# Performance work log

Measured on AMD Instinct MI355X. Metric: run time of the kernel, lower is better.

Reference implementation:

```python
import jax, jax.numpy as jnp
import numpy as np

B, M, FIN, K, FOUT, NNZ = 8, 40000, 64, 6, 64, 320000

def setup_inputs() -> dict:
    key = jax.random.key(0)
    k1, k2, k3, k4, k5 = jax.random.split(key, 5)
    x = jax.random.normal(k1, (B, M, FIN), dtype=jnp.float32)
    edge_rows = jax.random.randint(k2, (NNZ,), 0, M)
    edge_cols = jax.random.randint(k3, (NNZ,), 0, M)
    edge_vals = jax.random.normal(k4, (NNZ,), dtype=jnp.float32) * 0.1
    W = jax.random.normal(k5, (FIN * K, FOUT), dtype=jnp.float32) * 0.05
    return {"x": x, "edge_vals": edge_vals, "W": W,
            "edge_rows": edge_rows, "edge_cols": edge_cols}

def reference(x, edge_vals, W, edge_rows, edge_cols):
    Bd, Md, Fin = x.shape
    nK = W.shape[0] // Fin
    Fout = W.shape[1]
    # x0: [M, Fin*B] as in tf.transpose([1,2,0]) + reshape
    x0 = jnp.transpose(x, (1, 2, 0)).reshape(Md, Fin * Bd)

    def spmm_rescaled(v):
        # rescale_L(L, lmax=2) = L - I, so (L - I) @ v = L@v - v
        Lv = jax.ops.segment_sum(edge_vals[:, None] * v[edge_cols],
                                 edge_rows, num_segments=Md)
        return Lv - v

    xs = [x0]
    if nK > 1:
        x1 = spmm_rescaled(x0)
        xs.append(x1)
        xp, xc = x0, x1
        for _ in range(2, nK):
            xn = 2.0 * spmm_rescaled(xc) - xp  # Chebyshev recurrence
            xs.append(xn)
            xp, xc = xc, xn
    X = jnp.stack(xs, axis=0)                     # [K, M, Fin*B]
    X = X.reshape(nK, Md, Fin, Bd)                # split Fin*B -> (Fin, B)
    X = jnp.transpose(X, (3, 1, 2, 0))            # [B, M, Fin, K]
    X = X.reshape(Bd * Md, Fin * nK)
    out = (X @ W).reshape(Bd, Md, Fout)           # dense projection
    return out
```

## Files before the change

kernel.cpp:

```cpp
#include <hip/hip_runtime.h>

#define Mn    40000
#define Bn    8
#define FINn  64
#define Kn    6
#define FOUTn 64
#define NNZn  320000
#define Cn    512
#define NB    ((Mn + 255) / 256)
#define MT    (Mn / 64)


typedef _Float16 half8 __attribute__((ext_vector_type(8)));
typedef __attribute__((ext_vector_type(4))) float floatx4;

__device__ __forceinline__ ushort f2h(float f) {
    _Float16 h = (_Float16)f;
    return *(ushort*)&h;
}

__device__ __forceinline__ void gl_lds16(const ushort* g, ushort* l) {
    __builtin_amdgcn_global_load_lds(
        (const __attribute__((address_space(1))) unsigned int*)g,
        (__attribute__((address_space(3))) unsigned int*)l, 16, 0, 0);
}


__global__ __launch_bounds__(256) void k_hist(const int* __restrict__ rows,
                                              int* __restrict__ cnt) {
    int e = blockIdx.x * 256 + threadIdx.x;
    if (e < NNZn) atomicAdd(&cnt[rows[e]], 1);
}

__global__ __launch_bounds__(256) void k_scan_part(const int* __restrict__ cnt,
                                                   int* __restrict__ rowptr,
                                                   int* __restrict__ bsum) {
    __shared__ int part[256];
    int tid = threadIdx.x;
    int r = blockIdx.x * 256 + tid;
    int v = (r < Mn) ? cnt[r] : 0;
    part[tid] = v;
    __syncthreads();
    for (int off = 1; off < 256; off <<= 1) {
        int t = (tid >= off) ? part[tid - off] : 0;
        __syncthreads();
        part[tid] += t;
        __syncthreads();
    }
    if (r < Mn) rowptr[r] = part[tid] - v;
    if (tid == 255) bsum[blockIdx.x] = part[255];
}

__global__ __launch_bounds__(256) void k_scan_bsums(const int* __restrict__ bsum,
                                                    int* __restrict__ boff,
                                                    int* __restrict__ rowptr) {
    __shared__ int part[256];
    int tid = threadIdx.x;
    int v = (tid < NB) ? bsum[tid] : 0;
    part[tid] = v;
    __syncthreads();
    for (int off = 1; off < 256; off <<= 1) {
        int t = (tid >= off) ? part[tid - off] : 0;
        __syncthreads();
        part[tid] += t;
        __syncthreads();
    }
    if (tid < NB) boff[tid] = part[tid] - v;
    if (tid == 255) rowptr[Mn] = part[255];
}

__global__ __launch_bounds__(256) void k_scan_add(int* __restrict__ rowptr,
                                                  const int* __restrict__ boff,
                                                  int* __restrict__ wcur) {
    int r = blockIdx.x * 256 + threadIdx.x;
    if (r < Mn) {
        int v = rowptr[r] + boff[blockIdx.x];
        rowptr[r] = v;
        wcur[r] = v;
    }
}

__global__ __launch_bounds__(256) void k_scatter(const int* __restrict__ rows,
                                                 const int* __restrict__ cols,
                                                 const float* __restrict__ vals,
                                                 int* __restrict__ wcur,
                                                 int2* __restrict__ csr) {
    int e = blockIdx.x * 256 + threadIdx.x;
    if (e < NNZn) {
        int p = atomicAdd(&wcur[rows[e]], 1);
        int2 cv; cv.x = cols[e]; cv.y = __float_as_int(vals[e]);
        csr[p] = cv;
    }
}


__global__ __launch_bounds__(256) void k_transpose_h(const float* __restrict__ x,
                                                     ushort* __restrict__ x0h) {
    int m0 = blockIdx.x * 4;
    int t  = threadIdx.x;
#pragma unroll
    for (int k = 0; k < 2; ++k) {
        int i   = t + k * 256;
        int ml  = i >> 7;
        int rem = i & 127;
        int b   = rem >> 4;
        int fq  = (rem & 15) * 4;
        float4 a = *(const float4*)(x + ((size_t)b * Mn + m0 + ml) * 64 + fq);
        union { uint2 u; ushort h[4]; } s;
        s.h[0] = f2h(a.x); s.h[1] = f2h(a.y); s.h[2] = f2h(a.z); s.h[3] = f2h(a.w);
        *(uint2*)(x0h + (size_t)(m0 + ml) * Cn + b * 64 + fq) = s.u;
    }
}


__device__ __forceinline__ void fmah8(float* a, uint4 g, float w) {
    union { uint4 u; _Float16 h[8]; } c; c.u = g;
#pragma unroll
    for (int i = 0; i < 8; ++i) a[i] += w * (float)c.h[i];
}

__global__ __launch_bounds__(256) void k_spmm_h(const ushort* __restrict__ xc,
                                                const ushort* __restrict__ xp,
                                                ushort* __restrict__ xn,
                                                const int* __restrict__ rowptr,
                                                const int2* __restrict__ csr,
                                                int first) {
    int t = threadIdx.x;
    int lane = t & 63;
    int m = blockIdx.x * 4 + (t >> 6);
    const uint4* xc4 = (const uint4*)xc;
    uint4 v = xc4[(size_t)m * 64 + lane];
    uint4 p;
    if (!first) p = ((const uint4*)xp)[(size_t)m * 64 + lane];
    float a[8];
    { union { uint4 u; _Float16 h[8]; } c; c.u = v;
#pragma unroll
      for (int i = 0; i < 8; ++i) a[i] = -(float)c.h[i]; }

    int e = rowptr[m], end = rowptr[m + 1];
    for (; e + 8 <= end; e += 8) {
        int2 cv[8];
#pragma unroll
        for (int i = 0; i < 8; ++i) cv[i] = csr[e + i];
        uint4 g[8];
#pragma unroll
        for (int i = 0; i < 8; ++i) g[i] = xc4[(size_t)cv[i].x * 64 + lane];
#pragma unroll
        for (int i = 0; i < 8; ++i) fmah8(a, g[i], __int_as_float(cv[i].y));
    }
    for (; e + 4 <= end; e += 4) {
        int2 cv0 = csr[e],     cv1 = csr[e + 1];
        int2 cv2 = csr[e + 2], cv3 = csr[e + 3];
        uint4 g0 = xc4[(size_t)cv0.x * 64 + lane];
        uint4 g1 = xc4[(size_t)cv1.x * 64 + lane];
        uint4 g2 = xc4[(size_t)cv2.x * 64 + lane];
        uint4 g3 = xc4[(size_t)cv3.x * 64 + lane];
        fmah8(a, g0, __int_as_float(cv0.y));
        fmah8(a, g1, __int_as_float(cv1.y));
        fmah8(a, g2, __int_as_float(cv2.y));
        fmah8(a, g3, __int_as_float(cv3.y));
    }
    for (; e < end; ++e) {
        int2 cv = csr[e];
        uint4 g = xc4[(size_t)cv.x * 64 + lane];
        fmah8(a, g, __int_as_float(cv.y));
    }

    if (!first) {
        union { uint4 u; _Float16 h[8]; } c; c.u = p;
#pragma unroll
        for (int i = 0; i < 8; ++i) a[i] = 2.f * a[i] - (float)c.h[i];
    }
    union { uint4 u; _Float16 h[8]; } s;
#pragma unroll
    for (int i = 0; i < 8; ++i) s.h[i] = (_Float16)a[i];
    ((uint4*)xn)[(size_t)m * 64 + lane] = s.u;
}


__global__ __launch_bounds__(256) void k_wfrag(const float* __restrict__ W,
                                               ushort* __restrict__ wfrag) {
    int idx = blockIdx.x * 256 + threadIdx.x;
    if (idx >= 12 * 4 * 64 * 8) return;
    int j    = idx & 7;
    int lane = (idx >> 3) & 63;
    int n    = (idx >> 9) & 3;
    int kk   = idx >> 11;
    int k    = (lane >> 4) * 8 + j;
    int lev  = kk >> 1;
    int f    = (kk & 1) * 32 + k;
    int fo   = n * 16 + (lane & 15);
    wfrag[idx] = f2h(W[(f * Kn + lev) * FOUTn + fo]);
}


__global__ __launch_bounds__(256, 4) void k_gemm_mfma(const ushort* __restrict__ xh,
                                                      const ushort* __restrict__ wfrag,
                                                      float* __restrict__ out) {
    __shared__ __align__(16) ushort As[2][4][1024];
    int t     = threadIdx.x;
    int wv    = t >> 6;
    int lane  = t & 63;
    int q     = lane >> 4, r = lane & 15;
    int mtile = blockIdx.x % MT;
    int b     = blockIdx.x / MT;
    int m0    = mtile * 64;

    const size_t lstrideH = (size_t)Mn * Cn;

    int srow = lane >> 3;
    int gsw  = (lane & 7) ^ (srow & 7);
    const ushort* gsA = xh + (size_t)(m0 + wv * 16 + srow) * Cn + b * 64 + gsw * 8;
    const ushort* gsB = gsA + 8 * (size_t)Cn;
    int swz = r & 7;

    floatx4 acc0 = (floatx4)0.f, acc1 = (floatx4)0.f;
    floatx4 acc2 = (floatx4)0.f, acc3 = (floatx4)0.f;

#define STAGE(lev, buf) do {                                       \
        gl_lds16(gsA + (size_t)(lev) * lstrideH, &As[buf][wv][0]);   \
        gl_lds16(gsB + (size_t)(lev) * lstrideH, &As[buf][wv][512]); \
    } while (0)

#define MC(kkg, af) do {                                                              \
        const ushort* wf = wfrag + ((size_t)((kkg) * 4) * 64 + lane) * 8;             \
        acc0 = __builtin_amdgcn_mfma_f32_16x16x32_f16(af, *(const half8*)(wf),        acc0, 0, 0, 0); \
        acc1 = __builtin_amdgcn_mfma_f32_16x16x32_f16(af, *(const half8*)(wf + 512),  acc1, 0, 0, 0); \
        acc2 = __builtin_amdgcn_mfma_f32_16x16x32_f16(af, *(const half8*)(wf + 1024), acc2, 0, 0, 0); \
        acc3 = __builtin_amdgcn_mfma_f32_16x16x32_f16(af, *(const half8*)(wf + 1536), acc3, 0, 0, 0); \
    } while (0)

#define LEVEL(lev, buf, VMSTR) do {                                                   \
        asm volatile("s_waitcnt vmcnt(" VMSTR ")" ::: "memory");                      \
        __builtin_amdgcn_sched_barrier(0);                                            \
        half8 af0 = *(const half8*)&As[buf][wv][r * 64 + (((0 + q) ^ swz) << 3)];     \
        half8 af1 = *(const half8*)&As[buf][wv][r * 64 + (((4 + q) ^ swz) << 3)];     \
        asm volatile("s_waitcnt lgkmcnt(0)" ::: "memory");                            \
        __builtin_amdgcn_sched_barrier(0);                                            \
        if ((lev) < 4) STAGE((lev) + 2, buf);                                         \
        MC((lev) * 2, af0);                                                           \
        MC((lev) * 2 + 1, af1);                                                       \
    } while (0)

    STAGE(0, 0);
    STAGE(1, 1);
    LEVEL(0, 0, "2");
    LEVEL(1, 1, "2");
    LEVEL(2, 0, "2");
    LEVEL(3, 1, "2");
    LEVEL(4, 0, "2");
    LEVEL(5, 1, "0");

#undef LEVEL
#undef MC
#undef STAGE

    size_t obase = ((size_t)b * Mn + m0 + wv * 16) * FOUTn;
#pragma unroll
    for (int n = 0; n < 4; ++n) {
        floatx4 av = (n == 0) ? acc0 : (n == 1) ? acc1 : (n == 2) ? acc2 : acc3;
#pragma unroll
        for (int reg = 0; reg < 4; ++reg) {
            int orow = q * 4 + reg;
            out[obase + (size_t)orow * FOUTn + n * 16 + r] = av[reg];
        }
    }
}


__global__ __launch_bounds__(512) void k_transpose_f(const float* __restrict__ x,
                                                     float* __restrict__ x0) {
    int m = blockIdx.x, t = threadIdx.x;
    int b = t >> 6, f = t & 63;
    x0[(size_t)m * Cn + t] = x[((size_t)b * Mn + m) * 64 + f];
}

__global__ __launch_bounds__(256) void k_spmm_f32(const float4* __restrict__ xc,
                                                  const float4* __restrict__ xp,
                                                  float4* __restrict__ xn,
                                                  const int* __restrict__ rowptr,
                                                  const int2* __restrict__ csr,
                                                  int first) {
    int t = threadIdx.x;
    int lane = t & 63;
    int m = blockIdx.x * 4 + (t >> 6);
    size_t rb = (size_t)m * 128;
    float4 v0 = xc[rb + lane];
    float4 v1 = xc[rb + 64 + lane];
    float4 a0 = make_float4(-v0.x, -v0.y, -v0.z, -v0.w);
    float4 a1 = make_float4(-v1.x, -v1.y, -v1.z, -v1.w);
    int e = rowptr[m], end = rowptr[m + 1];
    for (; e < end; ++e) {
        int2 cv = csr[e];
        float w = __int_as_float(cv.y);
        const float4* r = xc + (size_t)cv.x * 128;
        float4 g0 = r[lane], g1 = r[64 + lane];
        a0.x += w * g0.x; a0.y += w * g0.y; a0.z += w * g0.z; a0.w += w * g0.w;
        a1.x += w * g1.x; a1.y += w * g1.y; a1.z += w * g1.z; a1.w += w * g1.w;
    }
    if (!first) {
        float4 p0 = xp[rb + lane];
        float4 p1 = xp[rb + 64 + lane];
        a0.x = 2.f * a0.x - p0.x; a0.y = 2.f * a0.y - p0.y;
        a0.z = 2.f * a0.z - p0.z; a0.w = 2.f * a0.w - p0.w;
        a1.x = 2.f * a1.x - p1.x; a1.y = 2.f * a1.y - p1.y;
        a1.z = 2.f * a1.z - p1.z; a1.w = 2.f * a1.w - p1.w;
    }
    xn[rb + lane] = a0;
    xn[rb + 64 + lane] = a1;
}

__global__ __launch_bounds__(256) void k_gemm2(const float* __restrict__ xa,
                                               const float* __restrict__ xb,
                                               const float* __restrict__ W,
                                               float* __restrict__ out,
                                               int ka, int kb, int accum) {
    __shared__ __align__(16) float Wa[64 * 64];
    __shared__ __align__(16) float Wb[64 * 64];
    __shared__ __align__(16) float xsa[4 * Cn];
    __shared__ __align__(16) float xsb[4 * Cn];
    int t = threadIdx.x;
    size_t m0 = (size_t)blockIdx.x * 4;
    for (int i = t; i < 4096; i += 256) {
        int f = i >> 6, fo = i & 63;
        Wa[i] = W[(f * Kn + ka) * FOUTn + fo];
        Wb[i] = W[(f * Kn + kb) * FOUTn + fo];
    }
    for (int i = t; i < 4 * Cn; i += 256) {
        xsa[i] = xa[m0 * Cn + i];
        xsb[i] = xb[m0 * Cn + i];
    }
    __syncthreads();
    int fo  = (t & 15) * 4;
    int idx = t >> 4;
    int m   = idx & 3;
    int bq  = idx >> 2;
    float4 acc0 = make_float4(0.f, 0.f, 0.f, 0.f);
    float4 acc1 = make_float4(0.f, 0.f, 0.f, 0.f);
    for (int f = 0; f < 64; ++f) {
        float4 wa = *(const float4*)&Wa[f * 64 + fo];
        float a0 = xsa[m * Cn + bq * 64 + f];
        float a1 = xsa[m * Cn + (bq + 4) * 64 + f];
        acc0.x += a0 * wa.x; acc0.y += a0 * wa.y; acc0.z += a0 * wa.z; acc0.w += a0 * wa.w;
        acc1.x += a1 * wa.x; acc1.y += a1 * wa.y; acc1.z += a1 * wa.z; acc1.w += a1 * wa.w;
        float4 wb = *(const float4*)&Wb[f * 64 + fo];
        float b0 = xsb[m * Cn + bq * 64 + f];
        float b1 = xsb[m * Cn + (bq + 4) * 64 + f];
        acc0.x += b0 * wb.x; acc0.y += b0 * wb.y; acc0.z += b0 * wb.z; acc0.w += b0 * wb.w;
        acc1.x += b1 * wb.x; acc1.y += b1 * wb.y; acc1.z += b1 * wb.z; acc1.w += b1 * wb.w;
    }
    size_t o0 = (((size_t)bq * Mn) + (m0 + m)) * FOUTn + fo;
    size_t o1 = (((size_t)(bq + 4) * Mn) + (m0 + m)) * FOUTn + fo;
    float4* out4_0 = (float4*)&out[o0];
    float4* out4_1 = (float4*)&out[o1];
    if (accum) {
        float4 c0 = *out4_0, c1 = *out4_1;
        acc0.x += c0.x; acc0.y += c0.y; acc0.z += c0.z; acc0.w += c0.w;
        acc1.x += c1.x; acc1.y += c1.y; acc1.z += c1.z; acc1.w += c1.w;
    }
    *out4_0 = acc0;
    *out4_1 = acc1;
}


extern "C" void kernel_launch(void* const* d_in, const int* in_sizes, int n_in,
                              void* d_out, int out_size, void* d_ws, size_t ws_size,
                              hipStream_t stream) {
    const float* x         = (const float*)d_in[0];
    const float* edge_vals = (const float*)d_in[1];
    const float* W         = (const float*)d_in[2];
    const int*   edge_rows = (const int*)d_in[3];
    const int*   edge_cols = (const int*)d_in[4];
    float* out = (float*)d_out;

    char* ws = (char*)d_ws;
    const size_t bufB = (size_t)Mn * Cn * sizeof(float);
    const size_t bufH = (size_t)Mn * Cn * sizeof(ushort);
    const size_t wfB  = 12 * 4 * 64 * 8 * sizeof(ushort);
    const size_t csrB = (size_t)(Mn + 4 + Mn) * 4 + (size_t)NNZn * 8;

    const int spmm_grid = Mn / 4;
    const int gemm_grid = MT * 8;

    if (ws_size >= 6 * bufH + wfB + csrB) {
        ushort* xh  = (ushort*)ws;
        ushort* wfr = (ushort*)(ws + 6 * bufH);
        int*    rowptr = (int*)(ws + 6 * bufH + wfB);
        int*    fill   = rowptr + (Mn + 4);
        int2*   csr    = (int2*)(fill + Mn);
        int*    bsum   = (int*)csr;
        int*    boff   = bsum + 256;
        ushort* slot[6];
        for (int l = 0; l < 6; ++l) slot[l] = xh + (size_t)l * Mn * Cn;

        hipMemsetAsync(fill, 0, Mn * sizeof(int), stream);
        k_hist<<<(NNZn + 255) / 256, 256, 0, stream>>>(edge_rows, fill);
        k_scan_part<<<NB, 256, 0, stream>>>(fill, rowptr, bsum);
        k_scan_bsums<<<1, 256, 0, stream>>>(bsum, boff, rowptr);
        k_scan_add<<<NB, 256, 0, stream>>>(rowptr, boff, fill);
        k_scatter<<<(NNZn + 255) / 256, 256, 0, stream>>>(edge_rows, edge_cols,
                                                          edge_vals, fill, csr);
        k_wfrag<<<96, 256, 0, stream>>>(W, wfr);

        k_transpose_h<<<Mn / 4, 256, 0, stream>>>(x, slot[0]);
        k_spmm_h<<<spmm_grid, 256, 0, stream>>>(slot[0], slot[0], slot[1],
                                                rowptr, csr, 1);
        k_spmm_h<<<spmm_grid, 256, 0, stream>>>(slot[1], slot[0], slot[2],
                                                rowptr, csr, 0);
        k_spmm_h<<<spmm_grid, 256, 0, stream>>>(slot[2], slot[1], slot[3],
                                                rowptr, csr, 0);
        k_spmm_h<<<spmm_grid, 256, 0, stream>>>(slot[3], slot[2], slot[4],
                                                rowptr, csr, 0);
        k_spmm_h<<<spmm_grid, 256, 0, stream>>>(slot[4], slot[3], slot[5],
                                                rowptr, csr, 0);
        k_gemm_mfma<<<gemm_grid, 256, 0, stream>>>(xh, wfr, out);
    } else {
        float* buf0 = (float*)(ws);
        float* buf1 = (float*)(ws + bufB);
        float* buf2 = (float*)(ws + 2 * bufB);
        int*   rowptr = (int*)(ws + 3 * bufB);
        int*   fill   = rowptr + (Mn + 4);
        int2*  csr    = (int2*)(fill + Mn);
        int*   bsum   = (int*)csr;
        int*   boff   = bsum + 256;
        hipMemsetAsync(fill, 0, Mn * sizeof(int), stream);
        k_hist<<<(NNZn + 255) / 256, 256, 0, stream>>>(edge_rows, fill);
        k_scan_part<<<NB, 256, 0, stream>>>(fill, rowptr, bsum);
        k_scan_bsums<<<1, 256, 0, stream>>>(bsum, boff, rowptr);
        k_scan_add<<<NB, 256, 0, stream>>>(rowptr, boff, fill);
        k_scatter<<<(NNZn + 255) / 256, 256, 0, stream>>>(edge_rows, edge_cols,
                                                          edge_vals, fill, csr);
        k_transpose_f<<<Mn, 512, 0, stream>>>(x, buf0);
        k_spmm_f32<<<Mn / 4, 256, 0, stream>>>((const float4*)buf0, (const float4*)buf0,
                                               (float4*)buf1, rowptr, csr, 1);
        k_gemm2<<<Mn / 4, 256, 0, stream>>>(buf0, buf1, W, out, 0, 1, 0);
        k_spmm_f32<<<Mn / 4, 256, 0, stream>>>((const float4*)buf1, (const float4*)buf0,
                                               (float4*)buf2, rowptr, csr, 0);
        k_spmm_f32<<<Mn / 4, 256, 0, stream>>>((const float4*)buf2, (const float4*)buf1,
                                               (float4*)buf0, rowptr, csr, 0);
        k_gemm2<<<Mn / 4, 256, 0, stream>>>(buf2, buf0, W, out, 2, 3, 1);
        k_spmm_f32<<<Mn / 4, 256, 0, stream>>>((const float4*)buf0, (const float4*)buf2,
                                               (float4*)buf1, rowptr, csr, 0);
        k_spmm_f32<<<Mn / 4, 256, 0, stream>>>((const float4*)buf1, (const float4*)buf0,
                                               (float4*)buf2, rowptr, csr, 0);
        k_gemm2<<<Mn / 4, 256, 0, stream>>>(buf1, buf2, W, out, 4, 5, 1);
    }
}
```

Baseline: 540.4 us.

## Repartition GEMM waves by output column so weight fragments stay in registers

```diff
diff --git a/kernel.cpp b/kernel.cpp
--- a/kernel.cpp
+++ b/kernel.cpp
@@ -197,7 +197,7 @@
 __global__ __launch_bounds__(256, 4) void k_gemm_mfma(const ushort* __restrict__ xh,
                                                       const ushort* __restrict__ wfrag,
                                                       float* __restrict__ out) {
-    __shared__ __align__(16) ushort As[2][4][1024];
+    __shared__ __align__(16) ushort As[2][4096];
     int t     = threadIdx.x;
     int wv    = t >> 6;
     int lane  = t & 63;
@@ -205,64 +205,80 @@
     int mtile = blockIdx.x % MT;
     int b     = blockIdx.x / MT;
     int m0    = mtile * 64;
+    int swz   = r & 7;
 
     const size_t lstrideH = (size_t)Mn * Cn;
 
-    int srow = lane >> 3;
+    const ushort* wfb = wfrag + ((size_t)wv * 64 + lane) * 8;
+    half8 wf0  = *(const half8*)(wfb);
+    half8 wf1  = *(const half8*)(wfb + 1 * 2048);
+    half8 wf2  = *(const half8*)(wfb + 2 * 2048);
+    half8 wf3  = *(const half8*)(wfb + 3 * 2048);
+    half8 wf4  = *(const half8*)(wfb + 4 * 2048);
+    half8 wf5  = *(const half8*)(wfb + 5 * 2048);
+    half8 wf6  = *(const half8*)(wfb + 6 * 2048);
+    half8 wf7  = *(const half8*)(wfb + 7 * 2048);
+    half8 wf8  = *(const half8*)(wfb + 8 * 2048);
+    half8 wf9  = *(const half8*)(wfb + 9 * 2048);
+    half8 wf10 = *(const half8*)(wfb + 10 * 2048);
+    half8 wf11 = *(const half8*)(wfb + 11 * 2048);
+
+    int srow = wv * 8 + (lane >> 3);
     int gsw  = (lane & 7) ^ (srow & 7);
-    const ushort* gsA = xh + (size_t)(m0 + wv * 16 + srow) * Cn + b * 64 + gsw * 8;
-    const ushort* gsB = gsA + 8 * (size_t)Cn;
-    int swz = r & 7;
+    const ushort* gsA = xh + (size_t)(m0 + srow) * Cn + b * 64 + gsw * 8;
+    const ushort* gsB = gsA + 32 * (size_t)Cn;
 
     floatx4 acc0 = (floatx4)0.f, acc1 = (floatx4)0.f;
     floatx4 acc2 = (floatx4)0.f, acc3 = (floatx4)0.f;
 
-#define STAGE(lev, buf) do {                                       \
-        gl_lds16(gsA + (size_t)(lev) * lstrideH, &As[buf][wv][0]);   \
-        gl_lds16(gsB + (size_t)(lev) * lstrideH, &As[buf][wv][512]); \
+#define STAGE(lev, buf) do {                                          \
+        gl_lds16(gsA + (size_t)(lev) * lstrideH, &As[buf][wv * 512]); \
+        gl_lds16(gsB + (size_t)(lev) * lstrideH, &As[buf][2048 + wv * 512]); \
     } while (0)
 
-#define MC(kkg, af) do {                                                              \
-        const ushort* wf = wfrag + ((size_t)((kkg) * 4) * 64 + lane) * 8;             \
-        acc0 = __builtin_amdgcn_mfma_f32_16x16x32_f16(af, *(const half8*)(wf),        acc0, 0, 0, 0); \
-        acc1 = __builtin_amdgcn_mfma_f32_16x16x32_f16(af, *(const half8*)(wf + 512),  acc1, 0, 0, 0); \
-        acc2 = __builtin_amdgcn_mfma_f32_16x16x32_f16(af, *(const half8*)(wf + 1024), acc2, 0, 0, 0); \
-        acc3 = __builtin_amdgcn_mfma_f32_16x16x32_f16(af, *(const half8*)(wf + 1536), acc3, 0, 0, 0); \
-    } while (0)
-
-#define LEVEL(lev, buf, VMSTR) do {                                                   \
+#define AF(buf, sub, half) \
+    (*(const half8*)&As[buf][((sub) * 16 + r) * 64 + (((((half) * 4) + q) ^ swz) << 3)])
+
+#define LEVEL(lev, buf, VMSTR, WFA, WFB) do {                                         \
         asm volatile("s_waitcnt vmcnt(" VMSTR ")" ::: "memory");                      \
-        __builtin_amdgcn_sched_barrier(0);                                            \
-        half8 af0 = *(const half8*)&As[buf][wv][r * 64 + (((0 + q) ^ swz) << 3)];     \
-        half8 af1 = *(const half8*)&As[buf][wv][r * 64 + (((4 + q) ^ swz) << 3)];     \
-        asm volatile("s_waitcnt lgkmcnt(0)" ::: "memory");                            \
-        __builtin_amdgcn_sched_barrier(0);                                            \
+        __syncthreads();                                                              \
+        half8 a00 = AF(buf, 0, 0); half8 a10 = AF(buf, 1, 0);                         \
+        half8 a20 = AF(buf, 2, 0); half8 a30 = AF(buf, 3, 0);                         \
+        half8 a01 = AF(buf, 0, 1); half8 a11 = AF(buf, 1, 1);                         \
+        half8 a21 = AF(buf, 2, 1); half8 a31 = AF(buf, 3, 1);                         \
+        acc0 = __builtin_amdgcn_mfma_f32_16x16x32_f16(a00, WFA, acc0, 0, 0, 0);       \
+        acc1 = __builtin_amdgcn_mfma_f32_16x16x32_f16(a10, WFA, acc1, 0, 0, 0);       \
+        acc2 = __builtin_amdgcn_mfma_f32_16x16x32_f16(a20, WFA, acc2, 0, 0, 0);       \
+        acc3 = __builtin_amdgcn_mfma_f32_16x16x32_f16(a30, WFA, acc3, 0, 0, 0);       \
+        acc0 = __builtin_amdgcn_mfma_f32_16x16x32_f16(a01, WFB, acc0, 0, 0, 0);       \
+        acc1 = __builtin_amdgcn_mfma_f32_16x16x32_f16(a11, WFB, acc1, 0, 0, 0);       \
+        acc2 = __builtin_amdgcn_mfma_f32_16x16x32_f16(a21, WFB, acc2, 0, 0, 0);       \
+        acc3 = __builtin_amdgcn_mfma_f32_16x16x32_f16(a31, WFB, acc3, 0, 0, 0);       \
+        __syncthreads();                                                              \
         if ((lev) < 4) STAGE((lev) + 2, buf);                                         \
-        MC((lev) * 2, af0);                                                           \
-        MC((lev) * 2 + 1, af1);                                                       \
     } while (0)
 
     STAGE(0, 0);
     STAGE(1, 1);
-    LEVEL(0, 0, "2");
-    LEVEL(1, 1, "2");
-    LEVEL(2, 0, "2");
-    LEVEL(3, 1, "2");
-    LEVEL(4, 0, "2");
-    LEVEL(5, 1, "0");
+    LEVEL(0, 0, "2", wf0,  wf1);
+    LEVEL(1, 1, "2", wf2,  wf3);
+    LEVEL(2, 0, "2", wf4,  wf5);
+    LEVEL(3, 1, "2", wf6,  wf7);
+    LEVEL(4, 0, "2", wf8,  wf9);
+    LEVEL(5, 1, "0", wf10, wf11);
 
 #undef LEVEL
-#undef MC
+#undef AF
 #undef STAGE
 
-    size_t obase = ((size_t)b * Mn + m0 + wv * 16) * FOUTn;
-#pragma unroll
-    for (int n = 0; n < 4; ++n) {
-        floatx4 av = (n == 0) ? acc0 : (n == 1) ? acc1 : (n == 2) ? acc2 : acc3;
+#pragma unroll
+    for (int sub = 0; sub < 4; ++sub) {
+        floatx4 av = (sub == 0) ? acc0 : (sub == 1) ? acc1 : (sub == 2) ? acc2 : acc3;
 #pragma unroll
         for (int reg = 0; reg < 4; ++reg) {
-            int orow = q * 4 + reg;
-            out[obase + (size_t)orow * FOUTn + n * 16 + r] = av[reg];
+            size_t o = ((size_t)b * Mn + m0 + sub * 16 + q * 4 + reg) * FOUTn
+                     + wv * 16 + r;
+            out[o] = av[reg];
         }
     }
 }
```

Result: faster. 521.6 us (-3.5%).
